# Kernel tuning notes

Hardware: AMD Instinct MI355X
Metric: run time of the kernel (lower is better)

Reference implementation:

```python
import jax, jax.numpy as jnp
import numpy as np

B, N, F, H, OUT = 64, 512, 128, 256, 6


def setup_inputs() -> dict:
    key = jax.random.key(0)
    ks = jax.random.split(key, 20)
    s = 0.02
    inp = {
        "x": jax.random.normal(ks[0], (B * N, F), dtype=jnp.float32),
        "edge_index": jax.random.randint(ks[1], (2, 16), 0, B * N),
        "edge_weight": jax.random.uniform(ks[2], (16,), dtype=jnp.float32),
        "batch": jnp.repeat(jnp.arange(B, dtype=jnp.int64), N),
        "sigma": jax.random.uniform(ks[3], (1,), dtype=jnp.float32),
        "Wg": s * jax.random.normal(ks[4], (F, F)), "bg": jnp.zeros((F,)),
        "Wrel0": s * jax.random.normal(ks[5], (F, H)), "Wroot0": s * jax.random.normal(ks[6], (F, H)), "brel0": jnp.zeros((H,)),
        "Wrel1": s * jax.random.normal(ks[7], (H, H)), "Wroot1": s * jax.random.normal(ks[8], (H, H)), "brel1": jnp.zeros((H,)),
        "Wrel2": s * jax.random.normal(ks[9], (H, H)), "Wroot2": s * jax.random.normal(ks[10], (H, H)), "brel2": jnp.zeros((H,)),
        "W1": s * jax.random.normal(ks[11], (H, H)), "b1": jnp.zeros((H,)),
        "Wout": s * jax.random.normal(ks[12], (H, OUT)), "bout": jnp.zeros((OUT,)),
    }
    return inp


def _forward(x, sigma, Wg, bg, Wrel0, Wroot0, brel0, Wrel1, Wroot1, brel1,
             Wrel2, Wroot2, brel2, W1, b1, Wout, bout):
    # gdmLinear
    h = x @ Wg + bg                      # [B*N, F]
    hw = h.reshape(B, N, -1)             # to_dense_batch (equal-size windows)
    # pairwise squared distances per window -> Gaussian kernel
    sq = jnp.sum(hw * hw, axis=-1)       # [B, N]
    dist = jnp.maximum(sq[:, :, None] + sq[:, None, :]
                       - 2.0 * jnp.einsum('bnf,bmf->bnm', hw, hw), 0.0)
    A = jnp.exp(-dist / (2.0 * sigma[0] ** 2))   # [B, N, N], all > 0
    A = A * (1.0 - jnp.eye(N, dtype=A.dtype))    # nonzero extraction drops self-loops

    def conv(h, Wrel, Wroot, brel):
        # GraphConv: out_i = W_rel @ sum_j A[j,i] * h_j + b_rel + W_root @ h_i
        agg = jnp.einsum('bji,bjf->bif', A, h)
        return agg @ Wrel + brel + h @ Wroot

    h = hw
    h = jax.nn.relu(conv(h, Wrel0, Wroot0, brel0))
    h = jax.nn.relu(conv(h, Wrel1, Wroot1, brel1))
    h = conv(h, Wrel2, Wroot2, brel2)
    g = jnp.mean(h, axis=1)              # global_mean_pool (equal-size graphs)
    g = jax.nn.relu(g @ W1 + b1)
    return g @ Wout + bout               # [B, OUT]


def reference(x, edge_index, edge_weight, batch, sigma, Wg, bg,
              Wrel0, Wroot0, brel0, Wrel1, Wroot1, brel1,
              Wrel2, Wroot2, brel2, W1, b1, Wout, bout):
    # edge_index / edge_weight / batch inputs are recomputed internally by GdmGNN
    return _forward(x, sigma, Wg, bg, Wrel0, Wroot0, brel0, Wrel1, Wroot1, brel1,
                    Wrel2, Wroot2, brel2, W1, b1, Wout, bout)
```

## Files before the change

### kernel.cpp

```cpp
#include <hip/hip_runtime.h>
#include <math.h>

#define Bsz 64
#define Nn 512
#define Ff 128
#define Hh 256
#define OUTD 6
#define MTOT (Bsz * Nn)

typedef __bf16 bf16x8 __attribute__((ext_vector_type(8)));
typedef float f32x4 __attribute__((ext_vector_type(4)));
typedef int int4v __attribute__((ext_vector_type(4)));
typedef unsigned short ushort4v __attribute__((ext_vector_type(4)));

__device__ __forceinline__ unsigned short f2bf(float f) {
    unsigned u = __float_as_uint(f);
    u += 0x7FFFu + ((u >> 16) & 1u);
    return (unsigned short)(u >> 16);
}
__device__ __forceinline__ float bf2f(unsigned short s) {
    return __uint_as_float(((unsigned)s) << 16);
}

#define SWZ(r) (((r) ^ ((r) >> 2)) & 3)

__device__ __forceinline__ void async_ld16(const unsigned short* g, unsigned short* l) {
    __builtin_amdgcn_global_load_lds(
        (const __attribute__((address_space(1))) void*)g,
        (__attribute__((address_space(3))) void*)l,
        16, 0, 0);
}

#define LDH 40
#define TSZ (128 * 32)

__global__ __launch_bounds__(512) void gemm_ah(
    const unsigned short* __restrict__ HT, const unsigned short* __restrict__ Arows,
    unsigned short* __restrict__ agg,
    int F, long strideHT, long strideA, long strideC, int mTiles)
{
    int id = blockIdx.x;
    int bz = id & 63;
    int t = id >> 6;
    int bx = t % mTiles;
    int by = t / mTiles;

    HT += (long)bz * strideHT;
    Arows += (long)bz * strideA;
    agg += (long)bz * strideC;

    __shared__ unsigned short As[2 * TSZ];
    __shared__ unsigned short Bs[2 * TSZ];

    int tid = threadIdx.x;
    int lane = tid & 63;
    int wave = tid >> 6;
    int quad = lane >> 4, l16 = lane & 15;
    int wm = (wave >> 1) * 32, wn = (wave & 1) * 64;
    int m0 = bx * 128, n0 = by * 128;

    int sr = lane >> 2, sc = lane & 3;

    f32x4 acc[2][4] = {};

    auto issue = [&](int g) {
        int kk = g << 5;
        unsigned short* Ad = As + (g & 1) * TSZ;
        unsigned short* Bd = Bs + (g & 1) * TSZ;
        int r = wave * 16 + sr;
        int c = sc ^ SWZ(r);
        async_ld16(HT + (long)(m0 + r) * Nn + kk + c * 8, Ad + (wave * 16) * 32);
        async_ld16(Arows + (long)(n0 + r) * Nn + kk + c * 8, Bd + (wave * 16) * 32);
    };

    issue(0);
    for (int g = 0; g < (Nn >> 5); ++g) {
        __syncthreads();
        if (g + 1 < (Nn >> 5)) issue(g + 1);
        const unsigned short* Ab = As + (g & 1) * TSZ;
        const unsigned short* Bb = Bs + (g & 1) * TSZ;
        bf16x8 af[2], bfr[4];
        #pragma unroll
        for (int i = 0; i < 2; ++i) {
            int r = wm + i * 16 + l16;
            af[i] = *(const bf16x8*)&Ab[r * 32 + (quad ^ SWZ(r)) * 8];
        }
        #pragma unroll
        for (int j = 0; j < 4; ++j) {
            int r = wn + j * 16 + l16;
            bfr[j] = *(const bf16x8*)&Bb[r * 32 + (quad ^ SWZ(r)) * 8];
        }
        #pragma unroll
        for (int i = 0; i < 2; ++i)
            #pragma unroll
            for (int j = 0; j < 4; ++j)
                acc[i][j] = __builtin_amdgcn_mfma_f32_16x16x32_bf16(
                    af[i], bfr[j], acc[i][j], 0, 0, 0);
    }

    #pragma unroll
    for (int i = 0; i < 2; ++i) {
        int f = m0 + wm + i * 16 + quad * 4;
        #pragma unroll
        for (int j = 0; j < 4; ++j) {
            int node = n0 + wn + j * 16 + l16;
            f32x4 v = acc[i][j];
            ushort4v p;
            p[0] = f2bf(v[0]); p[1] = f2bf(v[1]); p[2] = f2bf(v[2]); p[3] = f2bf(v[3]);
            *(ushort4v*)&agg[(long)node * F + f] = p;
        }
    }
}

template<int POOL>
__global__ __launch_bounds__(512) void dense_t(
    const unsigned short* __restrict__ A0, const unsigned short* __restrict__ B0T,
    const unsigned short* __restrict__ A1, const unsigned short* __restrict__ B1T,
    const float* __restrict__ bias,
    unsigned short* __restrict__ outB, unsigned short* __restrict__ outT,
    const float* __restrict__ w, float* __restrict__ vpart, float* __restrict__ mpart,
    int K0, int K1, int relu)
{
    int m0 = blockIdx.x * 128;
    int n0 = blockIdx.y * 128;

    __shared__ unsigned short As[2 * TSZ];
    __shared__ unsigned short Bs[2 * TSZ];
    __shared__ float vred[128];
    __shared__ float mred[128];

    int tid = threadIdx.x;
    int lane = tid & 63;
    int wave = tid >> 6;
    int quad = lane >> 4, l16 = lane & 15;
    int wm = (wave >> 1) * 32, wn = (wave & 1) * 64;

    int sr = lane >> 2, sc = lane & 3;

    int T0 = K0 >> 5, T1 = K1 >> 5;
    int T = T0 + T1;

    f32x4 acc[2][4] = {};

    auto issue = [&](int g) {
        const unsigned short* Ag; const unsigned short* Bg; int Kg, kk;
        if (g < T0) { Ag = A0; Bg = B0T; Kg = K0; kk = g << 5; }
        else        { Ag = A1; Bg = B1T; Kg = K1; kk = (g - T0) << 5; }
        unsigned short* Ad = As + (g & 1) * TSZ;
        unsigned short* Bd = Bs + (g & 1) * TSZ;
        int r = wave * 16 + sr;
        int c = sc ^ SWZ(r);
        async_ld16(Ag + (long)(m0 + r) * Kg + kk + c * 8, Ad + (wave * 16) * 32);
        async_ld16(Bg + (long)(n0 + r) * Kg + kk + c * 8, Bd + (wave * 16) * 32);
    };

    issue(0);
    for (int g = 0; g < T; ++g) {
        __syncthreads();
        if (g + 1 < T) issue(g + 1);
        const unsigned short* Ab = As + (g & 1) * TSZ;
        const unsigned short* Bb = Bs + (g & 1) * TSZ;
        bf16x8 af[2], bfr[4];
        #pragma unroll
        for (int i = 0; i < 2; ++i) {
            int r = wm + i * 16 + l16;
            af[i] = *(const bf16x8*)&Ab[r * 32 + (quad ^ SWZ(r)) * 8];
        }
        #pragma unroll
        for (int j = 0; j < 4; ++j) {
            int r = wn + j * 16 + l16;
            bfr[j] = *(const bf16x8*)&Bb[r * 32 + (quad ^ SWZ(r)) * 8];
        }
        #pragma unroll
        for (int i = 0; i < 2; ++i)
            #pragma unroll
            for (int j = 0; j < 4; ++j)
                acc[i][j] = __builtin_amdgcn_mfma_f32_16x16x32_bf16(
                    af[i], bfr[j], acc[i][j], 0, 0, 0);
    }

    if (POOL) {
        if (tid < 128) { vred[tid] = 0.f; mred[tid] = 0.f; }
        __syncthreads();
    }

    #pragma unroll
    for (int i = 0; i < 2; ++i) {
        int lf = wm + i * 16 + quad * 4;
        int of = m0 + lf;
        float b0 = bias[of + 0], b1 = bias[of + 1];
        float b2 = bias[of + 2], b3 = bias[of + 3];
        float vp0 = 0.f, vp1 = 0.f, vp2 = 0.f, vp3 = 0.f;
        float mp0 = 0.f, mp1 = 0.f, mp2 = 0.f, mp3 = 0.f;
        #pragma unroll
        for (int j = 0; j < 4; ++j) {
            int node = n0 + wn + j * 16 + l16;
            f32x4 v = acc[i][j];
            float o0 = v[0] + b0, o1 = v[1] + b1, o2 = v[2] + b2, o3 = v[3] + b3;
            if (relu) {
                o0 = fmaxf(o0, 0.f); o1 = fmaxf(o1, 0.f);
                o2 = fmaxf(o2, 0.f); o3 = fmaxf(o3, 0.f);
            }
            ushort4v p;
            p[0] = f2bf(o0); p[1] = f2bf(o1); p[2] = f2bf(o2); p[3] = f2bf(o3);
            if (!POOL) {
                *(ushort4v*)&outB[(long)node * Hh + of] = p;
                if (outT) {
                    long base = ((long)(node >> 9) * Hh) * 512 + (node & 511);
                    outT[base + (long)(of + 0) * 512] = p[0];
                    outT[base + (long)(of + 1) * 512] = p[1];
                    outT[base + (long)(of + 2) * 512] = p[2];
                    outT[base + (long)(of + 3) * 512] = p[3];
                }
            } else {
                float wv = w[node];
                float h0v = bf2f(p[0]), h1v = bf2f(p[1]);
                float h2v = bf2f(p[2]), h3v = bf2f(p[3]);
                vp0 += wv * h0v; vp1 += wv * h1v; vp2 += wv * h2v; vp3 += wv * h3v;
                mp0 += h0v; mp1 += h1v; mp2 += h2v; mp3 += h3v;
            }
        }
        if (POOL) {
            #pragma unroll
            for (int m = 1; m < 16; m <<= 1) {
                vp0 += __shfl_xor(vp0, m); vp1 += __shfl_xor(vp1, m);
                vp2 += __shfl_xor(vp2, m); vp3 += __shfl_xor(vp3, m);
                mp0 += __shfl_xor(mp0, m); mp1 += __shfl_xor(mp1, m);
                mp2 += __shfl_xor(mp2, m); mp3 += __shfl_xor(mp3, m);
            }
            if (l16 == 0) {
                atomicAdd(&vred[lf + 0], vp0); atomicAdd(&vred[lf + 1], vp1);
                atomicAdd(&vred[lf + 2], vp2); atomicAdd(&vred[lf + 3], vp3);
                atomicAdd(&mred[lf + 0], mp0); atomicAdd(&mred[lf + 1], mp1);
                atomicAdd(&mred[lf + 2], mp2); atomicAdd(&mred[lf + 3], mp3);
            }
        }
    }
    if (POOL) {
        __syncthreads();
        if (tid < 128) {
            long o = (long)blockIdx.y * Hh + m0 + tid;
            vpart[o] = vred[tid];
            mpart[o] = mred[tid];
        }
    }
}

__global__ __launch_bounds__(256) void prep_h0(
    const float* __restrict__ x, const float* __restrict__ Wg,
    const float* __restrict__ bg,
    const float* __restrict__ Wrel0, const float* __restrict__ Wroot0,
    const float* __restrict__ Wrel1, const float* __restrict__ Wroot1,
    unsigned short* __restrict__ T0, unsigned short* __restrict__ T1,
    unsigned short* __restrict__ T2, unsigned short* __restrict__ T3,
    unsigned short* __restrict__ WgT,
    float* __restrict__ w,
    unsigned short* __restrict__ h0b, unsigned short* __restrict__ h0T,
    float* __restrict__ sqv)
{
    if (blockIdx.x < 960) {
        int idx = blockIdx.x * 256 + threadIdx.x;
        if (idx >= 212992) { w[idx - 212992] = 0.f; return; }
        if (idx >= 196608) {
            int e = idx - 196608;
            int o = e >> 7, i = e & 127;
            WgT[e] = f2bf(Wg[(long)i * 128 + o]);
            return;
        }
        const float* src; unsigned short* dst; int kin; int e;
        if      (idx <  32768) { src = Wrel0;  dst = T0; kin = 128; e = idx; }
        else if (idx <  65536) { src = Wroot0; dst = T1; kin = 128; e = idx - 32768; }
        else if (idx < 131072) { src = Wrel1;  dst = T2; kin = 256; e = idx - 65536; }
        else                   { src = Wroot1; dst = T3; kin = 256; e = idx - 131072; }
        int o = (kin == 128) ? (e >> 7) : (e >> 8);
        int i = e & (kin - 1);
        dst[e] = f2bf(src[(long)i * 256 + o]);
        return;
    }

    __shared__ unsigned short As[128 * LDH];
    __shared__ unsigned short Bs[128 * LDH];
    __shared__ float rsq[128];

    int tid = threadIdx.x;
    int lane = tid & 63;
    int wave = tid >> 6;
    int quad = lane >> 4, l16 = lane & 15;
    int wm = (wave >> 1) * 64, wn = (wave & 1) * 64;
    int m0 = (blockIdx.x - 960) * 128;

    f32x4 acc[4][4] = {};

    for (int k0 = 0; k0 < Ff; k0 += 32) {
        __syncthreads();
        #pragma unroll
        for (int l = 0; l < 2; ++l) {
            int idx = tid + l * 256;
            int r = idx >> 2, ch = idx & 3;
            const float* px = x + (long)(m0 + r) * Ff + k0 + ch * 8;
            float4 xa = *(const float4*)px;
            float4 xb = *(const float4*)(px + 4);
            ushort4v pa, pb;
            pa[0] = f2bf(xa.x); pa[1] = f2bf(xa.y); pa[2] = f2bf(xa.z); pa[3] = f2bf(xa.w);
            pb[0] = f2bf(xb.x); pb[1] = f2bf(xb.y); pb[2] = f2bf(xb.z); pb[3] = f2bf(xb.w);
            *(ushort4v*)&As[r * LDH + ch * 8] = pa;
            *(ushort4v*)&As[r * LDH + ch * 8 + 4] = pb;
            int kk = k0 + ch * 8;
            ushort4v qa, qb;
            #pragma unroll
            for (int u = 0; u < 4; ++u) qa[u] = f2bf(Wg[(long)(kk + u) * 128 + r]);
            #pragma unroll
            for (int u = 0; u < 4; ++u) qb[u] = f2bf(Wg[(long)(kk + 4 + u) * 128 + r]);
            *(ushort4v*)&Bs[r * LDH + ch * 8] = qa;
            *(ushort4v*)&Bs[r * LDH + ch * 8 + 4] = qb;
        }
        __syncthreads();
        bf16x8 af[4], bfr[4];
        #pragma unroll
        for (int i = 0; i < 4; ++i)
            af[i] = *(const bf16x8*)&As[(wm + i * 16 + l16) * LDH + quad * 8];
        #pragma unroll
        for (int j = 0; j < 4; ++j)
            bfr[j] = *(const bf16x8*)&Bs[(wn + j * 16 + l16) * LDH + quad * 8];
        #pragma unroll
        for (int i = 0; i < 4; ++i)
            #pragma unroll
            for (int j = 0; j < 4; ++j)
                acc[i][j] = __builtin_amdgcn_mfma_f32_16x16x32_bf16(
                    af[i], bfr[j], acc[i][j], 0, 0, 0);
    }

    if (tid < 128) rsq[tid] = 0.f;
    __syncthreads();

    #pragma unroll
    for (int i = 0; i < 4; ++i) {
        int lrow = wm + i * 16 + quad * 4;
        int mb = m0 + lrow;
        float rp0 = 0.f, rp1 = 0.f, rp2 = 0.f, rp3 = 0.f;
        #pragma unroll
        for (int j = 0; j < 4; ++j) {
            int n = wn + j * 16 + l16;
            f32x4 v = acc[i][j];
            float bv = bg[n];
            unsigned short s0 = f2bf(v[0] + bv), s1 = f2bf(v[1] + bv);
            unsigned short s2 = f2bf(v[2] + bv), s3 = f2bf(v[3] + bv);
            h0b[(long)(mb + 0) * Ff + n] = s0;
            h0b[(long)(mb + 1) * Ff + n] = s1;
            h0b[(long)(mb + 2) * Ff + n] = s2;
            h0b[(long)(mb + 3) * Ff + n] = s3;
            ushort4v p; p[0] = s0; p[1] = s1; p[2] = s2; p[3] = s3;
            long ti = ((long)(mb >> 9) * Ff + n) * 512 + (mb & 511);
            *(ushort4v*)&h0T[ti] = p;
            float f0 = bf2f(s0), f1 = bf2f(s1), f2 = bf2f(s2), f3 = bf2f(s3);
            rp0 += f0 * f0; rp1 += f1 * f1; rp2 += f2 * f2; rp3 += f3 * f3;
        }
        #pragma unroll
        for (int m = 1; m < 16; m <<= 1) {
            rp0 += __shfl_xor(rp0, m);
            rp1 += __shfl_xor(rp1, m);
            rp2 += __shfl_xor(rp2, m);
            rp3 += __shfl_xor(rp3, m);
        }
        if (l16 == 0) {
            atomicAdd(&rsq[lrow + 0], rp0);
            atomicAdd(&rsq[lrow + 1], rp1);
            atomicAdd(&rsq[lrow + 2], rp2);
            atomicAdd(&rsq[lrow + 3], rp3);
        }
    }
    __syncthreads();
    if (tid < 128) sqv[m0 + tid] = rsq[tid];
}

__global__ __launch_bounds__(512) void gram_A_mfma(
    const unsigned short* __restrict__ h0b, const float* __restrict__ sqv,
    const float* __restrict__ sigma, unsigned short* __restrict__ Aout,
    float* __restrict__ w)
{
    int id = blockIdx.x;
    int b = id & 63;
    int t = id >> 6;
    int i0 = (t & 3) * 128, j0 = (t >> 2) * 128;

    const unsigned short* H = h0b + (long)b * Nn * Ff;
    const float* SQ = sqv + (long)b * Nn;
    unsigned short* Ab = Aout + (long)b * Nn * Nn;

    __shared__ unsigned short Is[2 * TSZ];
    __shared__ unsigned short Js[2 * TSZ];
    __shared__ float rsum[128];

    int tid = threadIdx.x;
    int lane = tid & 63;
    int wave = tid >> 6;
    int quad = lane >> 4, l16 = lane & 15;
    int wm = (wave >> 1) * 32, wn = (wave & 1) * 64;

    int sr = lane >> 2, sc = lane & 3;

    f32x4 acc[2][4] = {};

    auto issue = [&](int g) {
        int kk = g << 5;
        unsigned short* Id = Is + (g & 1) * TSZ;
        unsigned short* Jd = Js + (g & 1) * TSZ;
        int r = wave * 16 + sr;
        int c = sc ^ SWZ(r);
        async_ld16(H + (long)(i0 + r) * Ff + kk + c * 8, Id + (wave * 16) * 32);
        async_ld16(H + (long)(j0 + r) * Ff + kk + c * 8, Jd + (wave * 16) * 32);
    };

    issue(0);
    for (int g = 0; g < (Ff >> 5); ++g) {
        __syncthreads();
        if (g + 1 < (Ff >> 5)) issue(g + 1);
        const unsigned short* Ib = Is + (g & 1) * TSZ;
        const unsigned short* Jb = Js + (g & 1) * TSZ;
        bf16x8 af[2], bfr[4];
        #pragma unroll
        for (int i = 0; i < 2; ++i) {
            int r = wm + i * 16 + l16;
            af[i] = *(const bf16x8*)&Ib[r * 32 + (quad ^ SWZ(r)) * 8];
        }
        #pragma unroll
        for (int j = 0; j < 4; ++j) {
            int r = wn + j * 16 + l16;
            bfr[j] = *(const bf16x8*)&Jb[r * 32 + (quad ^ SWZ(r)) * 8];
        }
        #pragma unroll
        for (int i = 0; i < 2; ++i)
            #pragma unroll
            for (int j = 0; j < 4; ++j)
                acc[i][j] = __builtin_amdgcn_mfma_f32_16x16x32_bf16(
                    af[i], bfr[j], acc[i][j], 0, 0, 0);
    }

    if (tid < 128) rsum[tid] = 0.f;
    __syncthreads();

    float s = sigma[0];
    float inv2s2 = 1.0f / (2.0f * s * s);
    #pragma unroll
    for (int i = 0; i < 2; ++i) {
        int lrow = wm + i * 16 + quad * 4;
        int rb = i0 + lrow;
        float rs0 = 0.f, rs1 = 0.f, rs2 = 0.f, rs3 = 0.f;
        #pragma unroll
        for (int j = 0; j < 4; ++j) {
            int c = j0 + wn + j * 16 + l16;
            float sqc = SQ[c];
            f32x4 v = acc[i][j];
            ushort4v pk;
            float av[4];
            #pragma unroll
            for (int r4 = 0; r4 < 4; ++r4) {
                int r = rb + r4;
                float d = fmaxf(SQ[r] + sqc - 2.0f * v[r4], 0.0f);
                unsigned short a = (r == c) ? (unsigned short)0
                                            : f2bf(__expf(-d * inv2s2));
                pk[r4] = a;
                av[r4] = bf2f(a);
            }
            *(ushort4v*)&Ab[(long)c * Nn + rb] = pk;
            rs0 += av[0]; rs1 += av[1]; rs2 += av[2]; rs3 += av[3];
        }
        #pragma unroll
        for (int m = 1; m < 16; m <<= 1) {
            rs0 += __shfl_xor(rs0, m);
            rs1 += __shfl_xor(rs1, m);
            rs2 += __shfl_xor(rs2, m);
            rs3 += __shfl_xor(rs3, m);
        }
        if (l16 == 0) {
            atomicAdd(&rsum[lrow + 0], rs0);
            atomicAdd(&rsum[lrow + 1], rs1);
            atomicAdd(&rsum[lrow + 2], rs2);
            atomicAdd(&rsum[lrow + 3], rs3);
        }
    }
    __syncthreads();
    if (tid < 128) atomicAdd(&w[(long)b * Nn + i0 + tid], rsum[tid]);
}

__global__ __launch_bounds__(256) void head_kernel(
    const float* __restrict__ vpart, const float* __restrict__ mpart,
    const float* __restrict__ Wrel2, const float* __restrict__ Wroot2,
    const float* __restrict__ brel2,
    const float* __restrict__ W1, const float* __restrict__ b1,
    const float* __restrict__ Wout, const float* __restrict__ bout,
    float* __restrict__ out)
{
    int b = blockIdx.x;
    int j = threadIdx.x;
    __shared__ float vs[Hh], ms[Hh], gs[Hh], g2[Hh];
    float vp = 0.f, mp = 0.f;
    #pragma unroll
    for (int p = 0; p < 4; ++p) {
        long o = ((long)(b * 4 + p)) * Hh + j;
        vp += vpart[o];
        mp += mpart[o];
    }
    vs[j] = vp * (1.0f / (float)Nn);
    ms[j] = mp * (1.0f / (float)Nn);
    __syncthreads();
    float s = brel2[j];
    for (int c = 0; c < Hh; ++c)
        s += vs[c] * Wrel2[c * Hh + j] + ms[c] * Wroot2[c * Hh + j];
    gs[j] = s;
    __syncthreads();
    float t = b1[j];
    for (int k = 0; k < Hh; ++k) t += gs[k] * W1[k * Hh + j];
    g2[j] = fmaxf(t, 0.f);
    __syncthreads();
    if (j < OUTD) {
        float s2 = bout[j];
        for (int k = 0; k < Hh; ++k) s2 += g2[k] * Wout[k * OUTD + j];
        out[b * OUTD + j] = s2;
    }
}

extern "C" void kernel_launch(void* const* d_in, const int* in_sizes, int n_in,
                              void* d_out, int out_size, void* d_ws, size_t ws_size,
                              hipStream_t stream) {
    const float* x      = (const float*)d_in[0];
    const float* sigma  = (const float*)d_in[4];
    const float* Wg     = (const float*)d_in[5];
    const float* bg     = (const float*)d_in[6];
    const float* Wrel0  = (const float*)d_in[7];
    const float* Wroot0 = (const float*)d_in[8];
    const float* brel0  = (const float*)d_in[9];
    const float* Wrel1  = (const float*)d_in[10];
    const float* Wroot1 = (const float*)d_in[11];
    const float* brel1  = (const float*)d_in[12];
    const float* Wrel2  = (const float*)d_in[13];
    const float* Wroot2 = (const float*)d_in[14];
    const float* brel2  = (const float*)d_in[15];
    const float* W1     = (const float*)d_in[16];
    const float* b1     = (const float*)d_in[17];
    const float* Wout   = (const float*)d_in[18];
    const float* bout   = (const float*)d_in[19];
    float* out = (float*)d_out;

    char* ws = (char*)d_ws;
    unsigned short* WgT  = (unsigned short*)(ws + 0);
    unsigned short* h0b  = (unsigned short*)(ws + 16777216);
    unsigned short* h0T  = (unsigned short*)(ws + 25165824);
    float*          sq   = (float*)(ws + 33554432);
    unsigned short* Aadj = (unsigned short*)(ws + 33685504);
    unsigned short* agg  = (unsigned short*)(ws + 67239936);
    unsigned short* h1b  = (unsigned short*)(ws + 84017152);
    unsigned short* h1T  = (unsigned short*)(ws + 100794368);
    unsigned short* WrelT0  = (unsigned short*)(ws + 167903232);
    unsigned short* WrootT0 = (unsigned short*)(ws + 167968768);
    unsigned short* WrelT1  = (unsigned short*)(ws + 168034304);
    unsigned short* WrootT1 = (unsigned short*)(ws + 168165376);
    float*          w     = (float*)(ws + 168558592);
    float*          vpart = (float*)(ws + 168689664);
    float*          mpart = (float*)(ws + 168951808);

    prep_h0<<<1216, 256, 0, stream>>>(x, Wg, bg, Wrel0, Wroot0, Wrel1, Wroot1,
                                      WrelT0, WrootT0, WrelT1, WrootT1, WgT,
                                      w, h0b, h0T, sq);

    gram_A_mfma<<<dim3(16 * Bsz, 1, 1), 512, 0, stream>>>(h0b, sq, sigma, Aadj, w);

    gemm_ah<<<dim3(4 * Bsz, 1, 1), 512, 0, stream>>>(
        h0T, Aadj, agg, Ff,
        (long)Ff * Nn, (long)Nn * Nn, (long)Nn * Ff, 1);
    dense_t<0><<<dim3(2, MTOT / 128), 512, 0, stream>>>(
        WrelT0, agg, WrootT0, h0b, brel0, h1b, h1T,
        nullptr, nullptr, nullptr, Ff, Ff, 1);

    gemm_ah<<<dim3(8 * Bsz, 1, 1), 512, 0, stream>>>(
        h1T, Aadj, agg, Hh,
        (long)Hh * Nn, (long)Nn * Nn, (long)Nn * Hh, 2);
    dense_t<1><<<dim3(2, MTOT / 128), 512, 0, stream>>>(
        WrelT1, agg, WrootT1, h1b, brel1, nullptr, nullptr,
        w, vpart, mpart, Hh, Hh, 1);

    head_kernel<<<Bsz, 256, 0, stream>>>(vpart, mpart, Wrel2, Wroot2, brel2,
                                         W1, b1, Wout, bout, out);
}
```

Baseline: 229.6 us.

## Fuse layer-0 aggregation and dense transform into one kernel via LDS-resident agg

Merges the layer-0 A^T·h aggregation GEMM and the following dense Wrel/Wroot GEMM into a single kernel per (graph, node-tile). The aggregated tile stays in padded shared memory instead of going out to global memory and back. The kernel also drops the unused WgT transpose from the prep kernel and splits the templated dense kernel into a pooling-only variant. This removes one launch and one global write/read of the agg buffer. In exchange the fused kernel uses more LDS per block, which may lower occupancy, and it runs only 256 blocks for the dense phase.

```diff
diff --git a/kernel.cpp b/kernel.cpp
--- a/kernel.cpp
+++ b/kernel.cpp
@@ -33,6 +33,7 @@
 
 #define LDH 40
 #define TSZ (128 * 32)
+#define AGP 136
 
 __global__ __launch_bounds__(512) void gemm_ah(
     const unsigned short* __restrict__ HT, const unsigned short* __restrict__ Arows,
@@ -112,14 +113,167 @@
     }
 }
 
-template<int POOL>
-__global__ __launch_bounds__(512) void dense_t(
+__global__ __launch_bounds__(512) void fused_l0(
+    const unsigned short* __restrict__ h0T,
+    const unsigned short* __restrict__ Arows,
+    const unsigned short* __restrict__ h0b,
+    const unsigned short* __restrict__ WrelT0,
+    const unsigned short* __restrict__ WrootT0,
+    const float* __restrict__ brel0,
+    unsigned short* __restrict__ h1b,
+    unsigned short* __restrict__ h1T)
+{
+    int id = blockIdx.x;
+    int b = id & 63;
+    int nt = id >> 6;
+    int n0g = nt * 128;
+    long nodeBase = (long)b * Nn + n0g;
+
+    const unsigned short* HT = h0T + (long)b * Ff * Nn;
+    const unsigned short* AR = Arows + (long)b * Nn * Nn;
+
+    __shared__ unsigned short SA[2 * TSZ];
+    __shared__ unsigned short SB[2 * TSZ];
+    __shared__ unsigned short aggL[128 * AGP];
+
+    int tid = threadIdx.x;
+    int lane = tid & 63;
+    int wave = tid >> 6;
+    int quad = lane >> 4, l16 = lane & 15;
+    int wm = (wave >> 1) * 32, wn = (wave & 1) * 64;
+    int sr = lane >> 2, sc = lane & 3;
+
+    {
+        f32x4 acc[2][4] = {};
+        auto issue = [&](int g) {
+            int kk = g << 5;
+            unsigned short* Ad = SA + (g & 1) * TSZ;
+            unsigned short* Bd = SB + (g & 1) * TSZ;
+            int r = wave * 16 + sr;
+            int c = sc ^ SWZ(r);
+            async_ld16(HT + (long)r * Nn + kk + c * 8, Ad + (wave * 16) * 32);
+            async_ld16(AR + (long)(n0g + r) * Nn + kk + c * 8, Bd + (wave * 16) * 32);
+        };
+        issue(0);
+        for (int g = 0; g < (Nn >> 5); ++g) {
+            __syncthreads();
+            if (g + 1 < (Nn >> 5)) issue(g + 1);
+            const unsigned short* Ab = SA + (g & 1) * TSZ;
+            const unsigned short* Bb = SB + (g & 1) * TSZ;
+            bf16x8 af[2], bfr[4];
+            #pragma unroll
+            for (int i = 0; i < 2; ++i) {
+                int r = wm + i * 16 + l16;
+                af[i] = *(const bf16x8*)&Ab[r * 32 + (quad ^ SWZ(r)) * 8];
+            }
+            #pragma unroll
+            for (int j = 0; j < 4; ++j) {
+                int r = wn + j * 16 + l16;
+                bfr[j] = *(const bf16x8*)&Bb[r * 32 + (quad ^ SWZ(r)) * 8];
+            }
+            #pragma unroll
+            for (int i = 0; i < 2; ++i)
+                #pragma unroll
+                for (int j = 0; j < 4; ++j)
+                    acc[i][j] = __builtin_amdgcn_mfma_f32_16x16x32_bf16(
+                        af[i], bfr[j], acc[i][j], 0, 0, 0);
+        }
+        #pragma unroll
+        for (int i = 0; i < 2; ++i) {
+            int f = wm + i * 16 + quad * 4;
+            #pragma unroll
+            for (int j = 0; j < 4; ++j) {
+                int nl = wn + j * 16 + l16;
+                f32x4 v = acc[i][j];
+                ushort4v p;
+                p[0] = f2bf(v[0]); p[1] = f2bf(v[1]);
+                p[2] = f2bf(v[2]); p[3] = f2bf(v[3]);
+                *(ushort4v*)&aggL[nl * AGP + f] = p;
+            }
+        }
+    }
+    __syncthreads();
+
+    for (int half = 0; half < 2; ++half) {
+        int m0 = half * 128;
+        f32x4 acc[2][4] = {};
+        auto issue = [&](int g) {
+            unsigned short* Ad = SA + (g & 1) * TSZ;
+            int r = wave * 16 + sr;
+            int c = sc ^ SWZ(r);
+            if (g < 4) {
+                async_ld16(WrelT0 + (long)(m0 + r) * Ff + (g << 5) + c * 8,
+                           Ad + (wave * 16) * 32);
+            } else {
+                async_ld16(WrootT0 + (long)(m0 + r) * Ff + ((g - 4) << 5) + c * 8,
+                           Ad + (wave * 16) * 32);
+                unsigned short* Bd = SB + (g & 1) * TSZ;
+                async_ld16(h0b + (nodeBase + r) * Ff + ((g - 4) << 5) + c * 8,
+                           Bd + (wave * 16) * 32);
+            }
+        };
+        issue(0);
+        for (int g = 0; g < 8; ++g) {
+            __syncthreads();
+            if (g + 1 < 8) issue(g + 1);
+            const unsigned short* Ab = SA + (g & 1) * TSZ;
+            bf16x8 af[2], bfr[4];
+            #pragma unroll
+            for (int i = 0; i < 2; ++i) {
+                int r = wm + i * 16 + l16;
+                af[i] = *(const bf16x8*)&Ab[r * 32 + (quad ^ SWZ(r)) * 8];
+            }
+            if (g < 4) {
+                #pragma unroll
+                for (int j = 0; j < 4; ++j) {
+                    int nl = wn + j * 16 + l16;
+                    bfr[j] = *(const bf16x8*)&aggL[nl * AGP + (g << 5) + quad * 8];
+                }
+            } else {
+                const unsigned short* Bb = SB + (g & 1) * TSZ;
+                #pragma unroll
+                for (int j = 0; j < 4; ++j) {
+                    int r = wn + j * 16 + l16;
+                    bfr[j] = *(const bf16x8*)&Bb[r * 32 + (quad ^ SWZ(r)) * 8];
+                }
+            }
+            #pragma unroll
+            for (int i = 0; i < 2; ++i)
+                #pragma unroll
+                for (int j = 0; j < 4; ++j)
+                    acc[i][j] = __builtin_amdgcn_mfma_f32_16x16x32_bf16(
+                        af[i], bfr[j], acc[i][j], 0, 0, 0);
+        }
+        #pragma unroll
+        for (int i = 0; i < 2; ++i) {
+            int of = m0 + wm + i * 16 + quad * 4;
+            float b0 = brel0[of + 0], b1 = brel0[of + 1];
+            float b2 = brel0[of + 2], b3 = brel0[of + 3];
+            #pragma unroll
+            for (int j = 0; j < 4; ++j) {
+                int nl = wn + j * 16 + l16;
+                f32x4 v = acc[i][j];
+                float o0 = fmaxf(v[0] + b0, 0.f), o1 = fmaxf(v[1] + b1, 0.f);
+                float o2 = fmaxf(v[2] + b2, 0.f), o3 = fmaxf(v[3] + b3, 0.f);
+                ushort4v p;
+                p[0] = f2bf(o0); p[1] = f2bf(o1); p[2] = f2bf(o2); p[3] = f2bf(o3);
+                *(ushort4v*)&h1b[(nodeBase + nl) * Hh + of] = p;
+                long base = ((long)b * Hh) * 512 + n0g + nl;
+                h1T[base + (long)(of + 0) * 512] = p[0];
+                h1T[base + (long)(of + 1) * 512] = p[1];
+                h1T[base + (long)(of + 2) * 512] = p[2];
+                h1T[base + (long)(of + 3) * 512] = p[3];
+            }
+        }
+    }
+}
+
+__global__ __launch_bounds__(512) void dense_pool(
     const unsigned short* __restrict__ A0, const unsigned short* __restrict__ B0T,
     const unsigned short* __restrict__ A1, const unsigned short* __restrict__ B1T,
     const float* __restrict__ bias,
-    unsigned short* __restrict__ outB, unsigned short* __restrict__ outT,
     const float* __restrict__ w, float* __restrict__ vpart, float* __restrict__ mpart,
-    int K0, int K1, int relu)
+    int K0, int K1)
 {
     int m0 = blockIdx.x * 128;
     int n0 = blockIdx.y * 128;
@@ -179,10 +333,8 @@
                     af[i], bfr[j], acc[i][j], 0, 0, 0);
     }
 
-    if (POOL) {
-        if (tid < 128) { vred[tid] = 0.f; mred[tid] = 0.f; }
-        __syncthreads();
-    }
+    if (tid < 128) { vred[tid] = 0.f; mred[tid] = 0.f; }
+    __syncthreads();
 
     #pragma unroll
     for (int i = 0; i < 2; ++i) {
@@ -196,53 +348,33 @@
         for (int j = 0; j < 4; ++j) {
             int node = n0 + wn + j * 16 + l16;
             f32x4 v = acc[i][j];
-            float o0 = v[0] + b0, o1 = v[1] + b1, o2 = v[2] + b2, o3 = v[3] + b3;
-            if (relu) {
-                o0 = fmaxf(o0, 0.f); o1 = fmaxf(o1, 0.f);
-                o2 = fmaxf(o2, 0.f); o3 = fmaxf(o3, 0.f);
-            }
-            ushort4v p;
-            p[0] = f2bf(o0); p[1] = f2bf(o1); p[2] = f2bf(o2); p[3] = f2bf(o3);
-            if (!POOL) {
-                *(ushort4v*)&outB[(long)node * Hh + of] = p;
-                if (outT) {
-                    long base = ((long)(node >> 9) * Hh) * 512 + (node & 511);
-                    outT[base + (long)(of + 0) * 512] = p[0];
-                    outT[base + (long)(of + 1) * 512] = p[1];
-                    outT[base + (long)(of + 2) * 512] = p[2];
-                    outT[base + (long)(of + 3) * 512] = p[3];
-                }
-            } else {
-                float wv = w[node];
-                float h0v = bf2f(p[0]), h1v = bf2f(p[1]);
-                float h2v = bf2f(p[2]), h3v = bf2f(p[3]);
-                vp0 += wv * h0v; vp1 += wv * h1v; vp2 += wv * h2v; vp3 += wv * h3v;
-                mp0 += h0v; mp1 += h1v; mp2 += h2v; mp3 += h3v;
-            }
-        }
-        if (POOL) {
-            #pragma unroll
-            for (int m = 1; m < 16; m <<= 1) {
-                vp0 += __shfl_xor(vp0, m); vp1 += __shfl_xor(vp1, m);
-                vp2 += __shfl_xor(vp2, m); vp3 += __shfl_xor(vp3, m);
-                mp0 += __shfl_xor(mp0, m); mp1 += __shfl_xor(mp1, m);
-                mp2 += __shfl_xor(mp2, m); mp3 += __shfl_xor(mp3, m);
-            }
-            if (l16 == 0) {
-                atomicAdd(&vred[lf + 0], vp0); atomicAdd(&vred[lf + 1], vp1);
-                atomicAdd(&vred[lf + 2], vp2); atomicAdd(&vred[lf + 3], vp3);
-                atomicAdd(&mred[lf + 0], mp0); atomicAdd(&mred[lf + 1], mp1);
-                atomicAdd(&mred[lf + 2], mp2); atomicAdd(&mred[lf + 3], mp3);
-            }
-        }
-    }
-    if (POOL) {
-        __syncthreads();
-        if (tid < 128) {
-            long o = (long)blockIdx.y * Hh + m0 + tid;
-            vpart[o] = vred[tid];
-            mpart[o] = mred[tid];
-        }
+            float o0 = fmaxf(v[0] + b0, 0.f), o1 = fmaxf(v[1] + b1, 0.f);
+            float o2 = fmaxf(v[2] + b2, 0.f), o3 = fmaxf(v[3] + b3, 0.f);
+            float h0v = bf2f(f2bf(o0)), h1v = bf2f(f2bf(o1));
+            float h2v = bf2f(f2bf(o2)), h3v = bf2f(f2bf(o3));
+            float wv = w[node];
+            vp0 += wv * h0v; vp1 += wv * h1v; vp2 += wv * h2v; vp3 += wv * h3v;
+            mp0 += h0v; mp1 += h1v; mp2 += h2v; mp3 += h3v;
+        }
+        #pragma unroll
+        for (int m = 1; m < 16; m <<= 1) {
+            vp0 += __shfl_xor(vp0, m); vp1 += __shfl_xor(vp1, m);
+            vp2 += __shfl_xor(vp2, m); vp3 += __shfl_xor(vp3, m);
+            mp0 += __shfl_xor(mp0, m); mp1 += __shfl_xor(mp1, m);
+            mp2 += __shfl_xor(mp2, m); mp3 += __shfl_xor(mp3, m);
+        }
+        if (l16 == 0) {
+            atomicAdd(&vred[lf + 0], vp0); atomicAdd(&vred[lf + 1], vp1);
+            atomicAdd(&vred[lf + 2], vp2); atomicAdd(&vred[lf + 3], vp3);
+            atomicAdd(&mred[lf + 0], mp0); atomicAdd(&mred[lf + 1], mp1);
+            atomicAdd(&mred[lf + 2], mp2); atomicAdd(&mred[lf + 3], mp3);
+        }
+    }
+    __syncthreads();
+    if (tid < 128) {
+        long o = (long)blockIdx.y * Hh + m0 + tid;
+        vpart[o] = vred[tid];
+        mpart[o] = mred[tid];
     }
 }
 
@@ -253,20 +385,13 @@
     const float* __restrict__ Wrel1, const float* __restrict__ Wroot1,
     unsigned short* __restrict__ T0, unsigned short* __restrict__ T1,
     unsigned short* __restrict__ T2, unsigned short* __restrict__ T3,
-    unsigned short* __restrict__ WgT,
     float* __restrict__ w,
     unsigned short* __restrict__ h0b, unsigned short* __restrict__ h0T,
     float* __restrict__ sqv)
 {
-    if (blockIdx.x < 960) {
+    if (blockIdx.x < 896) {
         int idx = blockIdx.x * 256 + threadIdx.x;
-        if (idx >= 212992) { w[idx - 212992] = 0.f; return; }
-        if (idx >= 196608) {
-            int e = idx - 196608;
-            int o = e >> 7, i = e & 127;
-            WgT[e] = f2bf(Wg[(long)i * 128 + o]);
-            return;
-        }
+        if (idx >= 196608) { w[idx - 196608] = 0.f; return; }
         const float* src; unsigned short* dst; int kin; int e;
         if      (idx <  32768) { src = Wrel0;  dst = T0; kin = 128; e = idx; }
         else if (idx <  65536) { src = Wroot0; dst = T1; kin = 128; e = idx - 32768; }
@@ -287,7 +412,7 @@
     int wave = tid >> 6;
     int quad = lane >> 4, l16 = lane & 15;
     int wm = (wave >> 1) * 64, wn = (wave & 1) * 64;
-    int m0 = (blockIdx.x - 960) * 128;
+    int m0 = (blockIdx.x - 896) * 128;
 
     f32x4 acc[4][4] = {};
 
@@ -543,7 +668,6 @@
     float* out = (float*)d_out;
 
     char* ws = (char*)d_ws;
-    unsigned short* WgT  = (unsigned short*)(ws + 0);
     unsigned short* h0b  = (unsigned short*)(ws + 16777216);
     unsigned short* h0T  = (unsigned short*)(ws + 25165824);
     float*          sq   = (float*)(ws + 33554432);
@@ -559,25 +683,21 @@
     float*          vpart = (float*)(ws + 168689664);
     float*          mpart = (float*)(ws + 168951808);
 
-    prep_h0<<<1216, 256, 0, stream>>>(x, Wg, bg, Wrel0, Wroot0, Wrel1, Wroot1,
-                                      WrelT0, WrootT0, WrelT1, WrootT1, WgT,
+    prep_h0<<<1152, 256, 0, stream>>>(x, Wg, bg, Wrel0, Wroot0, Wrel1, Wroot1,
+                                      WrelT0, WrootT0, WrelT1, WrootT1,
                                       w, h0b, h0T, sq);
 
     gram_A_mfma<<<dim3(16 * Bsz, 1, 1), 512, 0, stream>>>(h0b, sq, sigma, Aadj, w);
 
-    gemm_ah<<<dim3(4 * Bsz, 1, 1), 512, 0, stream>>>(
-        h0T, Aadj, agg, Ff,
-        (long)Ff * Nn, (long)Nn * Nn, (long)Nn * Ff, 1);
-    dense_t<0><<<dim3(2, MTOT / 128), 512, 0, stream>>>(
-        WrelT0, agg, WrootT0, h0b, brel0, h1b, h1T,
-        nullptr, nullptr, nullptr, Ff, Ff, 1);
+    fused_l0<<<dim3(4 * Bsz, 1, 1), 512, 0, stream>>>(
+        h0T, Aadj, h0b, WrelT0, WrootT0, brel0, h1b, h1T);
 
     gemm_ah<<<dim3(8 * Bsz, 1, 1), 512, 0, stream>>>(
         h1T, Aadj, agg, Hh,
         (long)Hh * Nn, (long)Nn * Nn, (long)Nn * Hh, 2);
-    dense_t<1><<<dim3(2, MTOT / 128), 512, 0, stream>>>(
-        WrelT1, agg, WrootT1, h1b, brel1, nullptr, nullptr,
-        w, vpart, mpart, Hh, Hh, 1);
+    dense_pool<<<dim3(2, MTOT / 128), 512, 0, stream>>>(
+        WrelT1, agg, WrootT1, h1b, brel1,
+        w, vpart, mpart, Hh, Hh);
 
     head_kernel<<<Bsz, 256, 0, stream>>>(vpart, mpart, Wrel2, Wroot2, brel2,
                                          W1, b1, Wout, bout, out);
```

Result: faster. 224.0 us (-2.5%).
